# Performance work log

Measured on AMD Instinct MI355X. Metric: run time of the kernel, lower is better.

## Reference

```python
import jax, jax.numpy as jnp
import numpy as np

B, A, D, F, O, NB = 64, 1024, 5, 256, 256, 6  # batch, max_atoms, max_degree, ishape, oshape, bond feat dim


def setup_inputs() -> dict:
    key = jax.random.key(0)
    k1, k2, k3, k4 = jax.random.split(key, 4)
    atoms = jax.random.normal(k1, (B, A, F), dtype=jnp.float32)
    bonds = jax.random.normal(k2, (B, A, D, NB), dtype=jnp.float32)
    # -1 marks missing neighbor (degree padding); valid indices in [0, A)
    edges = jax.random.randint(k3, (B, A, D), -1, A)
    # xavier-normal-ish init for the 6 degree-specific weights, stacked [6, F+NB, O]
    scale = (2.0 / (F + NB + O)) ** 0.5
    degW = jax.random.normal(k4, (6, F + NB, O), dtype=jnp.float32) * scale
    b = jnp.full((1, O), 0.01, dtype=jnp.float32)
    return {"atoms": atoms, "bonds": bonds, "edges": edges, "degW": degW, "b": b}


def reference(atoms, bonds, edges, degW, b):
    # atoms: [B, A, F]; bonds: [B, A, D, NB]; edges: [B, A, D] int (-1 = pad)
    degrees = (edges != -1).sum(-1, keepdims=True)  # [B, A, 1]
    # pad a zero row at index 0 so edge -1 -> 0 gathers the mask value 0
    padded = jnp.pad(atoms, ((0, 0), (1, 0), (0, 0)))  # [B, A+1, F]
    neigh = jax.vmap(lambda p, e: p[e])(padded, edges + 1)  # [B, A, D, F]
    summed_atom = atoms + neigh.sum(axis=2)  # include_self=True
    feats = jnp.concatenate([summed_atom, bonds.sum(axis=2)], axis=-1)  # [B, A, F+NB]
    out = jnp.zeros((atoms.shape[0], atoms.shape[1], degW.shape[-1]), atoms.dtype)
    for d in range(6):  # fixed small structural loop over degree buckets
        mask = (degrees == d).astype(atoms.dtype)  # [B, A, 1]
        out = out + jax.nn.sigmoid(feats @ degW[d] + b) * mask
    return out
```

## Files before the change

kernel.cpp:

```cpp
#include <hip/hip_runtime.h>
#include <cstdint>

#define BATCH  64
#define NATOMS 1024
#define DEG    5
#define FIN    256
#define OOUT   256
#define NBF    6
#define KDIM   262
#define KP     288
#define NKT    9
#define MROWS  (BATCH * NATOMS)
#define MT     32
#define AS     296

typedef __attribute__((ext_vector_type(8))) short bf16x8;
typedef __attribute__((ext_vector_type(4))) float f32x4;

__device__ __forceinline__ unsigned short f2bf(float x) {
    unsigned u = __float_as_uint(x);
    u += 0x7fff + ((u >> 16) & 1);
    return (unsigned short)(u >> 16);
}
__device__ __forceinline__ float bf2f(unsigned short h) {
    return __uint_as_float(((unsigned)h) << 16);
}
__device__ __forceinline__ float sigmoidf_(float x) {
    return 1.f / (1.f + __expf(-x));
}

__global__ __launch_bounds__(256)
void convert_w_kernel(const float* __restrict__ degW, unsigned short* __restrict__ Wsw)
{
    const int idx = blockIdx.x * 256 + threadIdx.x;
    if (idx >= 16 * NKT * 64) return;
    const int lane = idx & 63;
    const int t    = (idx >> 6) % NKT;
    const int g    = (idx >> 6) / NKT;
    const int col  = g * 16 + (lane & 15);
    const int k0   = t * 32 + (lane >> 4) * 8;
    const float* __restrict__ W5 = degW + (size_t)DEG * KDIM * OOUT;
    unsigned short* dst = Wsw + (size_t)idx * 8;
    #pragma unroll
    for (int j = 0; j < 8; ++j) {
        const int k = k0 + j;
        dst[j] = f2bf((k < KDIM) ? W5[(size_t)k * OOUT + col] : 0.f);
    }
}

__global__ __launch_bounds__(256, 4)
void nfp_fused_kernel(const float* __restrict__ atoms, const float* __restrict__ bonds,
                      const int* __restrict__ edges, const unsigned short* __restrict__ Wsw,
                      const float* __restrict__ degW, const float* __restrict__ bias,
                      float* __restrict__ out)
{
    __shared__ short Afeat[MT * AS];
    __shared__ int   edg[MT * DEG];
    __shared__ int   deg_lds[MT];

    const int tid  = threadIdx.x;
    const int lane = tid & 63;
    const int wave = tid >> 6;

    const int bid   = blockIdx.x;
    const int xcd   = bid & 7;
    const int per   = bid >> 3;
    const int batch = (per >> 5) * 8 + xcd;
    const int blk   = per & 31;
    const int row0  = batch * NATOMS + blk * MT;

    if (tid < MT * DEG) edg[tid] = edges[row0 * DEG + tid];
    __syncthreads();
    if (tid < MT) {
        int dc = 0;
        #pragma unroll
        for (int d = 0; d < DEG; ++d) dc += (edg[tid * DEG + d] != -1) ? 1 : 0;
        deg_lds[tid] = dc;
    }

    const float* __restrict__ abase = atoms + ((size_t)batch << 10) * FIN;
    const int selfrow = blk * MT;
    #pragma unroll
    for (int c = 0; c < 4; ++c) {
        const int mb = wave * 8 + c * 2;
        float4 self[2];
        float4 nv[2][DEG];
        #pragma unroll
        for (int r = 0; r < 2; ++r) {
            const int m = mb + r;
            self[r] = *(const float4*)&abase[(size_t)(selfrow + m) * FIN + lane * 4];
            #pragma unroll
            for (int d = 0; d < DEG; ++d) {
                const int e  = edg[m * DEG + d];
                const int ei = (e >= 0) ? e : 0;
                nv[r][d] = *(const float4*)&abase[(size_t)ei * FIN + lane * 4];
            }
        }
        #pragma unroll
        for (int r = 0; r < 2; ++r) {
            const int m = mb + r;
            float4 v = self[r];
            #pragma unroll
            for (int d = 0; d < DEG; ++d) {
                const float fl = (edg[m * DEG + d] >= 0) ? 1.f : 0.f;
                v.x += fl * nv[r][d].x; v.y += fl * nv[r][d].y;
                v.z += fl * nv[r][d].z; v.w += fl * nv[r][d].w;
            }
            ushort4 us;
            us.x = f2bf(v.x); us.y = f2bf(v.y); us.z = f2bf(v.z); us.w = f2bf(v.w);
            *(ushort4*)&Afeat[m * AS + lane * 4] = us;
        }
    }
    #pragma unroll
    for (int i = lane; i < 8 * 32; i += 64) {
        const int r  = i >> 5, kk = i & 31;
        const int m  = wave * 8 + r;
        float bv = 0.f;
        if (kk < NBF) {
            const float* bb = bonds + ((size_t)row0 + m) * (DEG * NBF) + kk;
            bv = bb[0] + bb[NBF] + bb[2 * NBF] + bb[3 * NBF] + bb[4 * NBF];
        }
        Afeat[m * AS + FIN + kk] = f2bf(bv);
    }
    __syncthreads();

    const int fr = lane & 15;
    const int q  = lane >> 4;
    const int wn = wave * 64;

    f32x4 acc[2][4];
    #pragma unroll
    for (int i = 0; i < 2; ++i)
        #pragma unroll
        for (int j = 0; j < 4; ++j)
            acc[i][j] = (f32x4){0.f, 0.f, 0.f, 0.f};

    bf16x8 bcur[4], bnxt[4];
    #pragma unroll
    for (int j = 0; j < 4; ++j)
        bcur[j] = *(const bf16x8*)&Wsw[((size_t)((wave * 4 + j) * NKT) * 64 + lane) * 8];

    #pragma unroll
    for (int t = 0; t < NKT; ++t) {
        if (t + 1 < NKT) {
            #pragma unroll
            for (int j = 0; j < 4; ++j)
                bnxt[j] = *(const bf16x8*)&Wsw[((size_t)((wave * 4 + j) * NKT + t + 1) * 64 + lane) * 8];
        }
        bf16x8 af[2];
        #pragma unroll
        for (int i = 0; i < 2; ++i)
            af[i] = *(const bf16x8*)&Afeat[(i * 16 + fr) * AS + t * 32 + q * 8];
        #pragma unroll
        for (int i = 0; i < 2; ++i)
            #pragma unroll
            for (int j = 0; j < 4; ++j)
                acc[i][j] = __builtin_amdgcn_mfma_f32_16x16x32_bf16(af[i], bcur[j], acc[i][j], 0, 0, 0);
        #pragma unroll
        for (int j = 0; j < 4; ++j) bcur[j] = bnxt[j];
    }

    #pragma unroll
    for (int j = 0; j < 4; ++j) {
        const int gn = wn + j * 16 + fr;
        const float bj = bias[gn];
        #pragma unroll
        for (int i = 0; i < 2; ++i) {
            #pragma unroll
            for (int r = 0; r < 4; ++r) {
                const int lm = i * 16 + q * 4 + r;
                if (deg_lds[lm] == DEG)
                    __builtin_nontemporal_store(sigmoidf_(acc[i][j][r] + bj),
                                                &out[((size_t)row0 + lm) * OOUT + gn]);
            }
        }
    }

    for (int m = 0; m < MT; ++m) {
        const int dg = deg_lds[m];
        if (dg == DEG) continue;
        const float* __restrict__ W = degW + (size_t)dg * KDIM * OOUT;
        float s0 = 0.f, s1 = 0.f, s2 = 0.f, s3 = 0.f;
        #pragma unroll 2
        for (int k = 0; k < 260; k += 4) {
            const float w0 = W[(size_t)(k + 0) * OOUT + tid];
            const float w1 = W[(size_t)(k + 1) * OOUT + tid];
            const float w2 = W[(size_t)(k + 2) * OOUT + tid];
            const float w3 = W[(size_t)(k + 3) * OOUT + tid];
            s0 += bf2f(Afeat[m * AS + k + 0]) * w0;
            s1 += bf2f(Afeat[m * AS + k + 1]) * w1;
            s2 += bf2f(Afeat[m * AS + k + 2]) * w2;
            s3 += bf2f(Afeat[m * AS + k + 3]) * w3;
        }
        s0 += bf2f(Afeat[m * AS + 260]) * W[(size_t)260 * OOUT + tid];
        s1 += bf2f(Afeat[m * AS + 261]) * W[(size_t)261 * OOUT + tid];
        const float x = ((s0 + s1) + (s2 + s3)) + bias[tid];
        out[((size_t)row0 + m) * OOUT + tid] = sigmoidf_(x);
    }
}

#define FMT  32
#define FKT  32
#define FKPAD 288
__global__ __launch_bounds__(256, 2)
void nfp_conv_fallback(const float* __restrict__ atoms, const float* __restrict__ bonds,
                       const int* __restrict__ edges, const float* __restrict__ degW,
                       const float* __restrict__ bias, float* __restrict__ out)
{
    __shared__ float feats[FMT * FKPAD];
    __shared__ float wtile[FKT * OOUT];
    __shared__ int   edg[FMT * DEG];
    __shared__ int   deg_lds[FMT];
    __shared__ int   odd_list[FMT];
    __shared__ int   odd_cnt;
    __shared__ float b_lds[OOUT];

    const int tid = threadIdx.x, bid = blockIdx.x;
    const int batch = bid >> 5, a0 = (bid & 31) * FMT;
    const size_t atom_base = (size_t)batch * NATOMS;

    b_lds[tid] = bias[tid];
    if (tid == 0) odd_cnt = 0;
    if (tid < FMT * DEG) {
        const int m = tid / DEG, d = tid % DEG;
        edg[tid] = edges[(atom_base + a0 + m) * DEG + d];
    }
    __syncthreads();
    if (tid < FMT) {
        int dc = 0;
        #pragma unroll
        for (int d = 0; d < DEG; ++d) dc += (edg[tid * DEG + d] != -1) ? 1 : 0;
        deg_lds[tid] = dc;
        if (dc != DEG) { const int idx = atomicAdd(&odd_cnt, 1); odd_list[idx] = tid; }
    }
    __syncthreads();
    {
        const int f = tid;
        for (int m = 0; m < FMT; ++m) {
            float v = atoms[(atom_base + a0 + m) * FIN + f];
            #pragma unroll
            for (int d = 0; d < DEG; ++d) {
                const int e = edg[m * DEG + d];
                if (e >= 0) v += atoms[(atom_base + e) * FIN + f];
            }
            feats[m * FKPAD + f] = v;
        }
        #pragma unroll
        for (int t = 0; t < 4; ++t) {
            const int idx = t * 256 + tid;
            const int m = idx >> 5, kk = idx & 31;
            float v = 0.f;
            if (kk < NBF) {
                const size_t bb = (atom_base + a0 + m) * (size_t)(DEG * NBF);
                #pragma unroll
                for (int d = 0; d < DEG; ++d) v += bonds[bb + d * NBF + kk];
            }
            feats[m * FKPAD + FIN + kk] = v;
        }
    }
    const float* __restrict__ W5 = degW + (size_t)DEG * KDIM * OOUT;
    float acc[4][8];
    #pragma unroll
    for (int i = 0; i < 4; ++i)
        #pragma unroll
        for (int j = 0; j < 8; ++j) acc[i][j] = 0.f;
    const int tx = tid & 31, ty = tid >> 5;
    for (int kt = 0; kt < FKPAD; kt += FKT) {
        __syncthreads();
        #pragma unroll
        for (int t = 0; t < FKT; ++t) {
            const int k = kt + t;
            wtile[t * OOUT + tid] = (k < KDIM) ? W5[(size_t)k * OOUT + tid] : 0.f;
        }
        __syncthreads();
        #pragma unroll 4
        for (int r = 0; r < FKT; ++r) {
            float a_frag[4];
            #pragma unroll
            for (int i = 0; i < 4; ++i) a_frag[i] = feats[(ty * 4 + i) * FKPAD + kt + r];
            float w_frag[8];
            #pragma unroll
            for (int j = 0; j < 8; ++j) w_frag[j] = wtile[r * OOUT + tx + j * 32];
            #pragma unroll
            for (int i = 0; i < 4; ++i)
                #pragma unroll
                for (int j = 0; j < 8; ++j) acc[i][j] += a_frag[i] * w_frag[j];
        }
    }
    #pragma unroll
    for (int i = 0; i < 4; ++i) {
        const int m = ty * 4 + i;
        if (deg_lds[m] == DEG) {
            const size_t row = (atom_base + a0 + m) * (size_t)OOUT;
            #pragma unroll
            for (int j = 0; j < 8; ++j) {
                const int o = tx + j * 32;
                out[row + o] = sigmoidf_(acc[i][j] + b_lds[o]);
            }
        }
    }
    const int ocnt = odd_cnt;
    for (int i = 0; i < ocnt; ++i) {
        const int m = odd_list[i], d = deg_lds[m];
        const float* __restrict__ W = degW + (size_t)d * KDIM * OOUT;
        float a2 = 0.f;
        for (int k = 0; k < KDIM; ++k) a2 += feats[m * FKPAD + k] * W[(size_t)k * OOUT + tid];
        const size_t row = (atom_base + a0 + m) * (size_t)OOUT;
        out[row + tid] = sigmoidf_(a2 + b_lds[tid]);
    }
}

extern "C" void kernel_launch(void* const* d_in, const int* in_sizes, int n_in,
                              void* d_out, int out_size, void* d_ws, size_t ws_size,
                              hipStream_t stream) {
    const float* atoms = (const float*)d_in[0];
    const float* bonds = (const float*)d_in[1];
    const int*   edges = (const int*)d_in[2];
    const float* degW  = (const float*)d_in[3];
    const float* bias  = (const float*)d_in[4];
    float* out = (float*)d_out;

    const size_t WSW_BYTES = (size_t)16 * NKT * 64 * 8 * 2;

    if (ws_size < WSW_BYTES) {
        nfp_conv_fallback<<<BATCH * (NATOMS / FMT), 256, 0, stream>>>(
            atoms, bonds, edges, degW, bias, out);
        return;
    }

    unsigned short* Wsw = (unsigned short*)d_ws;
    convert_w_kernel<<<(16 * NKT * 64 + 255) / 256, 256, 0, stream>>>(degW, Wsw);
    nfp_fused_kernel<<<MROWS / MT, 256, 0, stream>>>(
        atoms, bonds, edges, Wsw, degW, bias, out);
}
```

Measured before the change: 198.3 us.

## Pre-convert atoms to bf16 and gather bf16 rows with zero-row padding

Adds a pre-pass that converts the fp32 atom features to bf16 in workspace, with an extra zero row for missing neighbours. The fused kernel then gathers self and neighbour rows as bf16, four rows at a time, and prefetches the first weight tiles earlier. It also lowers the occupancy hint in launch bounds. The aim is to halve gather bytes and raise loads in flight. The cost is an extra full conversion pass over the atoms and slightly more rounding error.

```diff
diff --git a/kernel.cpp b/kernel.cpp
--- a/kernel.cpp
+++ b/kernel.cpp
@@ -30,6 +30,18 @@
 }
 
 __global__ __launch_bounds__(256)
+void convert_atoms_kernel(const float* __restrict__ atoms, unsigned short* __restrict__ atomsb)
+{
+    const size_t i = (size_t)blockIdx.x * 256 + threadIdx.x;
+    const float4 v = ((const float4*)atoms)[i];
+    ushort4 us;
+    us.x = f2bf(v.x); us.y = f2bf(v.y); us.z = f2bf(v.z); us.w = f2bf(v.w);
+    ((ushort4*)atomsb)[i] = us;
+    if (blockIdx.x == 0 && threadIdx.x < 64)
+        ((uint2*)(atomsb + (size_t)MROWS * FIN))[threadIdx.x] = (uint2){0u, 0u};
+}
+
+__global__ __launch_bounds__(256)
 void convert_w_kernel(const float* __restrict__ degW, unsigned short* __restrict__ Wsw)
 {
     const int idx = blockIdx.x * 256 + threadIdx.x;
@@ -48,8 +60,9 @@
     }
 }
 
-__global__ __launch_bounds__(256, 4)
-void nfp_fused_kernel(const float* __restrict__ atoms, const float* __restrict__ bonds,
+__global__ __launch_bounds__(256, 2)
+void nfp_fused_kernel(const unsigned short* __restrict__ atomsb,
+                      const float* __restrict__ bonds,
                       const int* __restrict__ edges, const unsigned short* __restrict__ Wsw,
                       const float* __restrict__ degW, const float* __restrict__ bias,
                       float* __restrict__ out)
@@ -78,37 +91,42 @@
         deg_lds[tid] = dc;
     }
 
-    const float* __restrict__ abase = atoms + ((size_t)batch << 10) * FIN;
-    const int selfrow = blk * MT;
-    #pragma unroll
-    for (int c = 0; c < 4; ++c) {
-        const int mb = wave * 8 + c * 2;
-        float4 self[2];
-        float4 nv[2][DEG];
-        #pragma unroll
-        for (int r = 0; r < 2; ++r) {
+    bf16x8 bcur[4], bnxt[4];
+    #pragma unroll
+    for (int j = 0; j < 4; ++j)
+        bcur[j] = *(const bf16x8*)&Wsw[((size_t)((wave * 4 + j) * NKT) * 64 + lane) * 8];
+
+    #pragma unroll
+    for (int c = 0; c < 2; ++c) {
+        const int mb = wave * 8 + c * 4;
+        int eidx[4][6];
+        #pragma unroll
+        for (int r = 0; r < 4; ++r) {
             const int m = mb + r;
-            self[r] = *(const float4*)&abase[(size_t)(selfrow + m) * FIN + lane * 4];
+            eidx[r][0] = row0 + m;
             #pragma unroll
             for (int d = 0; d < DEG; ++d) {
-                const int e  = edg[m * DEG + d];
-                const int ei = (e >= 0) ? e : 0;
-                nv[r][d] = *(const float4*)&abase[(size_t)ei * FIN + lane * 4];
-            }
-        }
-        #pragma unroll
-        for (int r = 0; r < 2; ++r) {
-            const int m = mb + r;
-            float4 v = self[r];
-            #pragma unroll
-            for (int d = 0; d < DEG; ++d) {
-                const float fl = (edg[m * DEG + d] >= 0) ? 1.f : 0.f;
-                v.x += fl * nv[r][d].x; v.y += fl * nv[r][d].y;
-                v.z += fl * nv[r][d].z; v.w += fl * nv[r][d].w;
+                const int e = edg[m * DEG + d];
+                eidx[r][d + 1] = (e >= 0) ? ((batch << 10) + e) : MROWS;
+            }
+        }
+        ushort4 ld[4][6];
+        #pragma unroll
+        for (int r = 0; r < 4; ++r)
+            #pragma unroll
+            for (int s = 0; s < 6; ++s)
+                ld[r][s] = *(const ushort4*)&atomsb[(size_t)eidx[r][s] * FIN + lane * 4];
+        #pragma unroll
+        for (int r = 0; r < 4; ++r) {
+            float x = 0.f, y = 0.f, z = 0.f, w = 0.f;
+            #pragma unroll
+            for (int s = 0; s < 6; ++s) {
+                x += bf2f(ld[r][s].x); y += bf2f(ld[r][s].y);
+                z += bf2f(ld[r][s].z); w += bf2f(ld[r][s].w);
             }
             ushort4 us;
-            us.x = f2bf(v.x); us.y = f2bf(v.y); us.z = f2bf(v.z); us.w = f2bf(v.w);
-            *(ushort4*)&Afeat[m * AS + lane * 4] = us;
+            us.x = f2bf(x); us.y = f2bf(y); us.z = f2bf(z); us.w = f2bf(w);
+            *(ushort4*)&Afeat[(mb + r) * AS + lane * 4] = us;
         }
     }
     #pragma unroll
@@ -134,11 +152,6 @@
         #pragma unroll
         for (int j = 0; j < 4; ++j)
             acc[i][j] = (f32x4){0.f, 0.f, 0.f, 0.f};
-
-    bf16x8 bcur[4], bnxt[4];
-    #pragma unroll
-    for (int j = 0; j < 4; ++j)
-        bcur[j] = *(const bf16x8*)&Wsw[((size_t)((wave * 4 + j) * NKT) * 64 + lane) * 8];
 
     #pragma unroll
     for (int t = 0; t < NKT; ++t) {
@@ -320,16 +333,22 @@
     const float* bias  = (const float*)d_in[4];
     float* out = (float*)d_out;
 
-    const size_t WSW_BYTES = (size_t)16 * NKT * 64 * 8 * 2;
-
-    if (ws_size < WSW_BYTES) {
+    const size_t ATOMSB_BYTES = (size_t)(MROWS + 1) * FIN * 2;
+    const size_t WSW_OFF      = ATOMSB_BYTES;
+    const size_t WSW_BYTES    = (size_t)16 * NKT * 64 * 8 * 2;
+    const size_t NEEDED       = WSW_OFF + WSW_BYTES;
+
+    if (ws_size < NEEDED) {
         nfp_conv_fallback<<<BATCH * (NATOMS / FMT), 256, 0, stream>>>(
             atoms, bonds, edges, degW, bias, out);
         return;
     }
 
-    unsigned short* Wsw = (unsigned short*)d_ws;
+    unsigned short* atomsb = (unsigned short*)d_ws;
+    unsigned short* Wsw    = (unsigned short*)((char*)d_ws + WSW_OFF);
+
+    convert_atoms_kernel<<<MROWS * FIN / 4 / 256, 256, 0, stream>>>(atoms, atomsb);
     convert_w_kernel<<<(16 * NKT * 64 + 255) / 256, 256, 0, stream>>>(degW, Wsw);
     nfp_fused_kernel<<<MROWS / MT, 256, 0, stream>>>(
-        atoms, bonds, edges, Wsw, degW, bias, out);
-}
+        atomsb, bonds, edges, Wsw, degW, bias, out);
+}
```

New measurement: 209.8 us. +5.8%, slower.
